# Performance work log

Measured on AMD Instinct MI355X. Metric: run time of the kernel, lower is better.

The kernel has to match this reference:

```python
import jax, jax.numpy as jnp
import numpy as np

OBS_LEN = 16; PRED_LEN = 25; N = 192; P = N * N; GH = GW = 8
IN_DIM = 2; OUT_DIM = 5; ENC = 64; DEC = 128
EMB = 32; DYN = 32; C1 = 64; C2 = 16; SOC = 3 * 3 * C2

def lrelu(x):
    return jnp.where(x >= 0, x, 0.1 * x)

def lstm_step(x, h, c, Wih, Whh, bih, bhh):
    # torch nn.LSTM gate order: i, f, g, o
    z = x @ Wih.T + h @ Whh.T + (bih + bhh)
    i, f, g, o = jnp.split(z, 4, axis=-1)
    c = jax.nn.sigmoid(f) * c + jax.nn.sigmoid(i) * jnp.tanh(g)
    h = jax.nn.sigmoid(o) * jnp.tanh(c)
    return h, c

def _indexed_lstm(frames, idxs, n_states, Wip, bip, Wih, Whh, bih, bhh):
    # per-frame gather of hidden/cell rows -> one LSTM step -> scatter back
    H0 = jnp.zeros((n_states, ENC), jnp.float32)
    C0 = jnp.zeros((n_states, ENC), jnp.float32)
    def step(carry, inp):
        Hs, Cs = carry
        frame, idx = inp
        h, c = Hs[idx], Cs[idx]                       # gather [M, ENC]
        emb = lrelu(frame @ Wip.T + bip)              # [M, EMB]
        h, c = lstm_step(emb, h, c, Wih, Whh, bih, bhh)
        return (Hs.at[idx].set(h), Cs.at[idx].set(c)), None  # scatter
    (Hs, _), _ = jax.lax.scan(step, (H0, C0), (frames, idxs))
    return Hs

def setup_inputs():
    key = jax.random.key(0)
    ks = jax.random.split(key, 16)
    def w(k, shape, fan):
        return (jax.random.normal(k, shape, jnp.float32) / np.sqrt(fan)).astype(jnp.float32)
    inp = {}
    inp['obs_traj'] = jax.random.normal(ks[0], (OBS_LEN, N, IN_DIM), jnp.float32)
    inp['obs_ngbrs_traj'] = jax.random.normal(ks[1], (OBS_LEN, P, IN_DIM), jnp.float32)
    inp['masks'] = jnp.ones((N, GH, GW, ENC), dtype=bool)  # fully occupied social grid
    inp['masks_idxs'] = jax.random.randint(ks[2], (N * GH * GW,), 0, P)
    inp['obs_traj_idxs'] = jnp.tile(jnp.arange(N), (OBS_LEN, 1))        # all nodes present each frame
    inp['obs_ngbrs_traj_idxs'] = jnp.tile(jnp.arange(P), (OBS_LEN, 1))  # all pair slots present
    inp['num_nodes'] = N
    inp['Wip'] = w(ks[3], (EMB, IN_DIM), IN_DIM); inp['bip'] = jnp.zeros((EMB,), jnp.float32)
    inp['Wih_e'] = w(ks[4], (4 * ENC, EMB), EMB); inp['Whh_e'] = w(ks[5], (4 * ENC, ENC), ENC)
    inp['bih_e'] = jnp.zeros((4 * ENC,), jnp.float32); inp['bhh_e'] = jnp.zeros((4 * ENC,), jnp.float32)
    inp['Wdyn'] = w(ks[6], (DYN, ENC), ENC); inp['bdyn'] = jnp.zeros((DYN,), jnp.float32)
    inp['Wc1'] = w(ks[7], (C1, ENC, 3, 3), ENC * 9); inp['bc1'] = jnp.zeros((C1,), jnp.float32)
    inp['Wc2'] = w(ks[8], (C2, C1, 3, 3), C1 * 9); inp['bc2'] = jnp.zeros((C2,), jnp.float32)
    inp['Wih_d'] = w(ks[9], (4 * DEC, SOC + DYN), SOC + DYN); inp['Whh_d'] = w(ks[10], (4 * DEC, DEC), DEC)
    inp['bih_d'] = jnp.zeros((4 * DEC,), jnp.float32); inp['bhh_d'] = jnp.zeros((4 * DEC,), jnp.float32)
    inp['Wop'] = w(ks[11], (OUT_DIM, DEC), DEC); inp['bop'] = jnp.zeros((OUT_DIM,), jnp.float32)
    return inp

def reference(obs_traj, obs_ngbrs_traj, masks, masks_idxs, obs_traj_idxs,
              obs_ngbrs_traj_idxs, num_nodes, Wip, bip, Wih_e, Whh_e, bih_e, bhh_e,
              Wdyn, bdyn, Wc1, bc1, Wc2, bc2, Wih_d, Whh_d, bih_d, bhh_d, Wop, bop):
    B = obs_traj_idxs.shape[1]
    # ego-trajectory encoder: per-frame indexed LSTM over num_nodes state slots
    Hs = _indexed_lstm(obs_traj, obs_traj_idxs, num_nodes, Wip, bip, Wih_e, Whh_e, bih_e, bhh_e)
    final_h = Hs[obs_traj_idxs[-1]]                   # [B, ENC]
    traj_enc = lrelu(final_h @ Wdyn.T + bdyn)         # [B, DYN]
    # neighbor-pair encoder: per-frame indexed LSTM over num_nodes^2 state slots
    Hn = _indexed_lstm(obs_ngbrs_traj, obs_ngbrs_traj_idxs, num_nodes * num_nodes,
                       Wip, bip, Wih_e, Whh_e, bih_e, bhh_e)
    ngbr_h = Hn[masks_idxs]                           # [B*GH*GW, ENC]
    # masked_scatter_ of neighbor encodings into fully-occupied social grid == reshape
    soc = jnp.where(masks, ngbr_h.reshape(B, GH, GW, ENC), 0.0)
    soc = jnp.transpose(soc, (0, 3, 2, 1))            # [B, ENC, GW, GH]
    dn = ('NCHW', 'OIHW', 'NCHW')
    soc = lrelu(jax.lax.conv_general_dilated(soc, Wc1, (1, 1), 'VALID', dimension_numbers=dn)
                + bc1[None, :, None, None])           # [B, C1, 6, 6]
    soc = lrelu(jax.lax.conv_general_dilated(soc, Wc2, (1, 1), 'VALID', dimension_numbers=dn)
                + bc2[None, :, None, None])           # [B, C2, 4, 4]
    soc = jax.lax.reduce_window(soc, -jnp.inf, jax.lax.max, (1, 1, 2, 2), (1, 1, 1, 1), 'VALID')
    soc = soc.reshape(B, SOC)                         # [B, 144]
    enc = jnp.concatenate([traj_enc, soc], axis=1)    # [B, DYN+SOC]
    h0 = jnp.zeros((B, DEC), jnp.float32); c0 = jnp.zeros((B, DEC), jnp.float32)
    def dec_step(carry, _):
        h, c = carry
        h, c = lstm_step(enc, h, c, Wih_d, Whh_d, bih_d, bhh_d)
        return (h, c), h
    _, hs = jax.lax.scan(dec_step, (h0, c0), None, length=PRED_LEN)
    o = hs @ Wop.T + bop                              # [PRED_LEN, B, 5]
    # bivariate Gaussian output activation (mu_x, mu_y, sigma_x, sigma_y, corr)
    return jnp.stack([o[..., 0], o[..., 1], jnp.exp(o[..., 2]),
                      jnp.exp(o[..., 3]), jnp.tanh(o[..., 4])], axis=-1)
```

## Files before the change

### kernel.cpp

```cpp
#include <hip/hip_runtime.h>
#include <hip/hip_bf16.h>

#define OBS_LEN 16
#define PRED_LEN 25
#define NNODES 192
#define PAIRS 36864
#define ENC 64
#define EMB 32
#define KTOT 96
#define DEC 128
#define SOCDYN 176
#define PAIR_GROUPS 2304
#define EGO_GROUPS 12
#define PREP_ELEMS 234496
#define HSTR 136

typedef short short8 __attribute__((ext_vector_type(8)));
typedef float f32x4 __attribute__((ext_vector_type(4)));

__device__ __forceinline__ float sigm(float x) {
    return __builtin_amdgcn_rcpf(1.f + __expf(-x));
}
__device__ __forceinline__ float tanh_f(float x) {
    return fmaf(-2.f, __builtin_amdgcn_rcpf(1.f + __expf(2.f * x)), 1.f);
}
__device__ __forceinline__ float lrelu(float x) { return (x >= 0.f) ? x : 0.1f * x; }

__device__ __forceinline__ unsigned short f2bf(float f) {
    union { float f; unsigned u; } v; v.f = f;
    unsigned r = v.u + 0x7fffu + ((v.u >> 16) & 1u);
    return (unsigned short)(r >> 16);
}
__device__ __forceinline__ float bf2f(unsigned short s) {
    union { unsigned u; float f; } v; v.u = ((unsigned)s) << 16; return v.f;
}

__global__ __launch_bounds__(1024, 1)
void prep_dedup_kernel(const float* __restrict__ Wih_d, const float* __restrict__ Whh_d,
                       const float* __restrict__ Wc1, const float* __restrict__ Wc2,
                       const float* __restrict__ Wih_e, const float* __restrict__ Whh_e,
                       const int* __restrict__ masks_idxs,
                       unsigned short* __restrict__ Whh_bf, unsigned short* __restrict__ Wih_bf,
                       unsigned short* __restrict__ WT1bf, unsigned short* __restrict__ WT2bf,
                       unsigned short* __restrict__ Wenc_bf,
                       int* __restrict__ list, int* __restrict__ list_count)
{
    const int t = threadIdx.x, b = blockIdx.x;
    if (b < 229) {
        int idx = b * 1024 + t;
        if (idx < 65536) {
            int m = idx >> 7, k = idx & 127;
            Whh_bf[idx] = f2bf(Whh_d[m * 128 + k]);
        } else if (idx < 65536 + 98304) {
            int i = idx - 65536;
            int m = i / 192, k = i % 192;
            Wih_bf[i] = (k < 176) ? f2bf(Wih_d[m * 176 + k]) : (unsigned short)0;
        } else if (idx < 65536 + 98304 + 36864) {
            int i = idx - (65536 + 98304);
            int o = i / 576, k = i % 576;
            int c = k / 9, tap = k % 9;
            WT1bf[i] = f2bf(Wc1[(o * 64 + c) * 9 + tap]);
        } else if (idx < 65536 + 98304 + 36864 + 9216) {
            int i = idx - (65536 + 98304 + 36864);
            int o = i / 576, k = i % 576;
            int c = k / 9, tap = k % 9;
            WT2bf[i] = f2bf(Wc2[(o * 64 + c) * 9 + tap]);
        } else if (idx < PREP_ELEMS) {
            int i = idx - (65536 + 98304 + 36864 + 9216);
            int m = i / 96, k = i % 96;
            Wenc_bf[i] = f2bf((k < 32) ? Wih_e[m * 32 + k] : Whh_e[m * 64 + (k - 32)]);
        }
        return;
    }
    __shared__ unsigned bm[1152];
    __shared__ int pcs[1024];
    for (int i = t; i < 1152; i += 1024) bm[i] = 0u;
    __syncthreads();
    for (int i = t; i < 12288; i += 1024) {
        const int r = masks_idxs[i];
        atomicOr(&bm[r >> 5], 1u << (r & 31));
    }
    __syncthreads();
    int pc = 0;
    if (t < 576) pc = __popc(bm[2 * t]) + __popc(bm[2 * t + 1]);
    pcs[t] = pc;
    __syncthreads();
    for (int ofs = 1; ofs < 1024; ofs <<= 1) {
        int v = (t >= ofs) ? pcs[t - ofs] : 0;
        __syncthreads();
        pcs[t] += v;
        __syncthreads();
    }
    if (t == 1023) list_count[0] = pcs[1023];
    if (t < 576) {
        int base = pcs[t] - pc;
#pragma unroll
        for (int wi = 0; wi < 2; ++wi) {
            unsigned wv = bm[2 * t + wi];
            const int rowbase = (2 * t + wi) * 32;
            while (wv) {
                const int bit = __ffs(wv) - 1;
                list[base++] = rowbase + bit;
                wv &= wv - 1;
            }
        }
    }
}

__global__ __launch_bounds__(256, 3)
void enc_lstm_kernel(const float* __restrict__ obs_traj,
                     const float* __restrict__ obs_ngbrs,
                     const float* __restrict__ Wip, const float* __restrict__ bip,
                     const unsigned short* __restrict__ Wenc_bf,
                     const float* __restrict__ bih, const float* __restrict__ bhh,
                     const int* __restrict__ list, const int* __restrict__ list_count,
                     float* __restrict__ Hn,
                     float* __restrict__ final_h)
{
    __shared__ __align__(16) short embs[16 * 16 * 40];
    __shared__ __align__(16) short hb[2][16 * 72];
    __shared__ int rows_s[16];

    const int t = threadIdx.x;
    const int wj = t >> 6, lane = t & 63, ln = lane & 15, kq = lane >> 4;
    const int b = blockIdx.x;
    const bool is_ego = (b >= PAIR_GROUPS);

    if (!is_ego) {
        const int cnt = list_count[0];
        if (b * 16 >= cnt) return;
        if (t < 16) rows_s[t] = list[min(b * 16 + t, cnt - 1)];
    } else {
        if (t < 16) rows_s[t] = (b - PAIR_GROUPS) * 16 + t;
    }

    short8 afrag[4][3];
#pragma unroll
    for (int g = 0; g < 4; ++g)
#pragma unroll
        for (int kc = 0; kc < 3; ++kc)
            afrag[g][kc] = *(const short8*)&Wenc_bf[(g * 64 + wj * 16 + ln) * 96 + kc * 32 + kq * 8];

    float bsv[4][4];
#pragma unroll
    for (int g = 0; g < 4; ++g)
#pragma unroll
        for (int r = 0; r < 4; ++r) {
            const int m = g * 64 + wj * 16 + kq * 4 + r;
            bsv[g][r] = bih[m] + bhh[m];
        }

    __syncthreads();

    {
        const int row = t & 15, stp = t >> 4;
        const int r = rows_s[row];
        const float* sp = is_ego ? (obs_traj + stp * NNODES * 2)
                                 : (obs_ngbrs + stp * PAIRS * 2);
        const float x0 = sp[r * 2 + 0];
        const float x1 = sp[r * 2 + 1];
        unsigned* dst = (unsigned*)&embs[(stp * 16 + row) * 40];
#pragma unroll
        for (int k = 0; k < 32; k += 2) {
            const float e0 = lrelu(fmaf(x0, Wip[2 * k + 0], fmaf(x1, Wip[2 * k + 1], bip[k])));
            const float e1 = lrelu(fmaf(x0, Wip[2 * k + 2], fmaf(x1, Wip[2 * k + 3], bip[k + 1])));
            dst[k >> 1] = (unsigned)f2bf(e0) | ((unsigned)f2bf(e1) << 16);
        }
    }
    for (int i = t; i < 2 * 16 * 72 / 2; i += 256) ((unsigned*)hb)[i] = 0u;
    __syncthreads();

    float cst[4] = {0.f, 0.f, 0.f, 0.f};
    int p = 0;
    for (int stp = 0; stp < OBS_LEN; ++stp) {
        const short8 bf0 = *(const short8*)&embs[(stp * 16 + ln) * 40 + kq * 8];
        const short* hbp = &hb[p][ln * 72 + kq * 8];
        const short8 bf1 = *(const short8*)hbp;
        const short8 bf2 = *(const short8*)(hbp + 32);
        f32x4 acc[4];
#pragma unroll
        for (int g = 0; g < 4; ++g) {
            f32x4 a = { bsv[g][0], bsv[g][1], bsv[g][2], bsv[g][3] };
            a = __builtin_amdgcn_mfma_f32_16x16x32_bf16(afrag[g][0], bf0, a, 0, 0, 0);
            a = __builtin_amdgcn_mfma_f32_16x16x32_bf16(afrag[g][1], bf1, a, 0, 0, 0);
            acc[g] = __builtin_amdgcn_mfma_f32_16x16x32_bf16(afrag[g][2], bf2, a, 0, 0, 0);
        }
        unsigned long long pk = 0;
#pragma unroll
        for (int r = 0; r < 4; ++r) {
            const float cn = fmaf(sigm(acc[1][r]), cst[r], sigm(acc[0][r]) * tanh_f(acc[2][r]));
            cst[r] = cn;
            const float h = sigm(acc[3][r]) * tanh_f(cn);
            pk |= (unsigned long long)f2bf(h) << (16 * r);
        }
        *(unsigned long long*)&hb[1 - p][ln * 72 + wj * 16 + kq * 4] = pk;
        p ^= 1;
        __syncthreads();
    }

    {
        const int row = t >> 4, k0 = (t & 15) * 4;
        unsigned long long pk = *(const unsigned long long*)&hb[p][row * 72 + k0];
        float4 v;
        v.x = bf2f((unsigned short)(pk));
        v.y = bf2f((unsigned short)(pk >> 16));
        v.z = bf2f((unsigned short)(pk >> 32));
        v.w = bf2f((unsigned short)(pk >> 48));
        float* dst = is_ego ? (final_h + rows_s[row] * 64 + k0)
                            : (Hn + (long)rows_s[row] * 64 + k0);
        *(float4*)dst = v;
    }
}

__global__ __launch_bounds__(256, 1)
void conv_kernel(const float* __restrict__ Hn, const int* __restrict__ masks_idxs,
                 const float* __restrict__ final_h, const float* __restrict__ Wdyn,
                 const float* __restrict__ bdyn,
                 const unsigned short* __restrict__ WT1bf, const float* __restrict__ bc1,
                 const unsigned short* __restrict__ WT2bf, const float* __restrict__ bc2,
                 float* __restrict__ enc)
{
    __shared__ __align__(16) short in2bf[64][72];
    __shared__ __align__(16) short imc1[48][584];
    __shared__ __align__(16) short s1bf[64][40];
    __shared__ __align__(16) short imc2[16][584];
    __shared__ __align__(16) float red[4][256];
    __shared__ float s2s[16 * 17];

    const int t = threadIdx.x, b = blockIdx.x;
    const int w = t >> 6, lane = t & 63, ln = lane & 15, kq = lane >> 4;

    short8 a1f[18];
#pragma unroll
    for (int kc = 0; kc < 18; ++kc)
        a1f[kc] = *(const short8*)&WT1bf[(w * 16 + ln) * 576 + kc * 32 + kq * 8];

    const int c2start = (w < 2) ? w * 5 : 10 + (w - 2) * 4;
    const int c2cnt = (w < 2) ? 5 : 4;
    short8 a2f[5];
#pragma unroll
    for (int i = 0; i < 5; ++i) {
        const int kc = c2start + min(i, c2cnt - 1);
        a2f[i] = *(const short8*)&WT2bf[ln * 576 + kc * 32 + kq * 8];
    }

    for (int i = 0; i < 16; ++i) {
        const int c = t & 63;
        const int p = (i << 2) + (t >> 6);
        const int u = p >> 3, v = p & 7;
        const int row = masks_idxs[b * 64 + v * 8 + u];
        in2bf[c][p] = (short)f2bf(Hn[(long)row * 64 + c]);
    }
    if (t < 32) {
        float acc = bdyn[t];
        for (int k = 0; k < 64; ++k) acc = fmaf(final_h[b * 64 + k], Wdyn[t * 64 + k], acc);
        enc[b * SOCDYN + t] = lrelu(acc);
    }
    __syncthreads();

    for (int i = t; i < 36 * 64; i += 256) {
        const int n = i >> 6, c = i & 63;
        const int x = n / 6, y = n % 6;
        short* dst = &imc1[n][c * 9];
#pragma unroll
        for (int dx = 0; dx < 3; ++dx)
#pragma unroll
            for (int dy = 0; dy < 3; ++dy)
                dst[dx * 3 + dy] = in2bf[c][(x + dx) * 8 + (y + dy)];
    }
    __syncthreads();

    {
        float bcv[4];
#pragma unroll
        for (int r = 0; r < 4; ++r) bcv[r] = bc1[w * 16 + kq * 4 + r];
#pragma unroll
        for (int nt = 0; nt < 3; ++nt) {
            f32x4 acc = { bcv[0], bcv[1], bcv[2], bcv[3] };
            const short* bp = &imc1[nt * 16 + ln][kq * 8];
#pragma unroll
            for (int kc = 0; kc < 18; ++kc) {
                const short8 bfr = *(const short8*)(bp + kc * 32);
                acc = __builtin_amdgcn_mfma_f32_16x16x32_bf16(a1f[kc], bfr, acc, 0, 0, 0);
            }
            const int n = nt * 16 + ln;
            if (n < 36) {
#pragma unroll
                for (int r = 0; r < 4; ++r)
                    s1bf[w * 16 + kq * 4 + r][n] = (short)f2bf(lrelu(acc[r]));
            }
        }
    }
    __syncthreads();

    for (int i = t; i < 16 * 64; i += 256) {
        const int n2 = i >> 6, c = i & 63;
        const int x = n2 >> 2, y = n2 & 3;
        short* dst = &imc2[n2][c * 9];
#pragma unroll
        for (int dx = 0; dx < 3; ++dx)
#pragma unroll
            for (int dy = 0; dy < 3; ++dy)
                dst[dx * 3 + dy] = s1bf[c][(x + dx) * 6 + (y + dy)];
    }
    __syncthreads();

    {
        f32x4 acc = { 0.f, 0.f, 0.f, 0.f };
        const short* bp = &imc2[ln][kq * 8];
#pragma unroll
        for (int i = 0; i < 5; ++i) {
            if (i < c2cnt) {
                const short8 bfr = *(const short8*)(bp + (c2start + i) * 32);
                acc = __builtin_amdgcn_mfma_f32_16x16x32_bf16(a2f[i], bfr, acc, 0, 0, 0);
            }
        }
        *(f32x4*)&red[w][lane * 4] = acc;
    }
    __syncthreads();

    {
        const float v = red[0][t] + red[1][t] + red[2][t] + red[3][t];
        const int l = t >> 2, r = t & 3;
        const int m = (l >> 4) * 4 + r, n = l & 15;
        s2s[m * 17 + n] = lrelu(v + bc2[m]);
    }
    __syncthreads();

    if (t < 144) {
        const int o = t / 9, ij = t % 9, i = ij / 3, j = ij % 3;
        const float v00 = s2s[o * 17 + i * 4 + j];
        const float v01 = s2s[o * 17 + i * 4 + j + 1];
        const float v10 = s2s[o * 17 + (i + 1) * 4 + j];
        const float v11 = s2s[o * 17 + (i + 1) * 4 + j + 1];
        enc[b * SOCDYN + 32 + t] = fmaxf(fmaxf(v00, v01), fmaxf(v10, v11));
    }
}

__global__ __launch_bounds__(512, 1)
void dec_kernel(const float* __restrict__ enc,
                const unsigned short* __restrict__ Wih_bf,
                const unsigned short* __restrict__ Whh_bf,
                const float* __restrict__ bih_d, const float* __restrict__ bhh_d,
                const float* __restrict__ Wop, const float* __restrict__ bop,
                float* __restrict__ out)
{
    __shared__ __align__(16) short encfr[3072];
    __shared__ __align__(16) short hist[PRED_LEN * 16 * HSTR];
    __shared__ float wop_s[5 * 128];

    const int t = threadIdx.x;
    const int w = t >> 6, lane = t & 63, ln = lane & 15, kq = lane >> 4;
    const int row0 = blockIdx.x * 16;

    for (int i = t; i < 3072; i += 512) {
        const int n = i / 192, k = i % 192;
        const float v = (k < 176) ? enc[(row0 + n) * SOCDYN + k] : 0.f;
        encfr[(k >> 3) * 128 + n * 8 + (k & 7)] = (short)f2bf(v);
    }
    for (int i = t; i < 640; i += 512) wop_s[i] = Wop[i];

    short8 wfrag[4][4];
#pragma unroll
    for (int g = 0; g < 4; ++g)
#pragma unroll
        for (int kc = 0; kc < 4; ++kc)
            wfrag[g][kc] = *(const short8*)&Whh_bf[(g * 128 + w * 16 + ln) * 128 + kc * 32 + kq * 8];

    f32x4 zin[4];
#pragma unroll
    for (int g = 0; g < 4; ++g)
#pragma unroll
        for (int r = 0; r < 4; ++r) {
            const int m = g * 128 + w * 16 + kq * 4 + r;
            zin[g][r] = bih_d[m] + bhh_d[m];
        }

    __syncthreads();

#pragma unroll
    for (int kc = 0; kc < 6; ++kc) {
        const short8 bfr = *(const short8*)&encfr[(kc * 4 + kq) * 128 + ln * 8];
#pragma unroll
        for (int g = 0; g < 4; ++g) {
            const short8 afr = *(const short8*)&Wih_bf[(g * 128 + w * 16 + ln) * 192 + kc * 32 + kq * 8];
            zin[g] = __builtin_amdgcn_mfma_f32_16x16x32_bf16(afr, bfr, zin[g], 0, 0, 0);
        }
    }

    float c4[4] = {0.f, 0.f, 0.f, 0.f};
    const int hb_wr = ln * HSTR + w * 16 + kq * 4;

    for (int stp = 0; stp < PRED_LEN; ++stp) {
        f32x4 z[4];
#pragma unroll
        for (int g = 0; g < 4; ++g) z[g] = zin[g];
        if (stp > 0) {
            const short* hp = &hist[(stp - 1) * 16 * HSTR + ln * HSTR + kq * 8];
            short8 bh[4];
#pragma unroll
            for (int kc = 0; kc < 4; ++kc)
                bh[kc] = *(const short8*)(hp + kc * 32);
#pragma unroll
            for (int kc = 0; kc < 4; ++kc)
#pragma unroll
                for (int g = 0; g < 4; ++g)
                    z[g] = __builtin_amdgcn_mfma_f32_16x16x32_bf16(wfrag[g][kc], bh[kc], z[g], 0, 0, 0);
        }
        unsigned long long pk = 0;
#pragma unroll
        for (int r = 0; r < 4; ++r) {
            const float cn = fmaf(sigm(z[1][r]), c4[r], sigm(z[0][r]) * tanh_f(z[2][r]));
            c4[r] = cn;
            const float h = sigm(z[3][r]) * tanh_f(cn);
            pk |= (unsigned long long)f2bf(h) << (16 * r);
        }
        *(unsigned long long*)&hist[stp * 16 * HSTR + hb_wr] = pk;
        __syncthreads();
    }

    for (int pi = t; pi < PRED_LEN * 16; pi += 512) {
        const int ts = pi >> 4, n = pi & 15;
        const short* hp = &hist[(ts * 16 + n) * HSTR];
        float a0 = bop[0], a1 = bop[1], a2 = bop[2], a3 = bop[3], a4 = bop[4];
#pragma unroll 4
        for (int kb = 0; kb < 16; ++kb) {
            const short8 h8 = *(const short8*)(hp + kb * 8);
#pragma unroll
            for (int q = 0; q < 8; ++q) {
                const float h = bf2f((unsigned short)h8[q]);
                const int k = kb * 8 + q;
                a0 = fmaf(h, wop_s[0 * 128 + k], a0);
                a1 = fmaf(h, wop_s[1 * 128 + k], a1);
                a2 = fmaf(h, wop_s[2 * 128 + k], a2);
                a3 = fmaf(h, wop_s[3 * 128 + k], a3);
                a4 = fmaf(h, wop_s[4 * 128 + k], a4);
            }
        }
        float* op = &out[((long)ts * NNODES + row0 + n) * 5];
        op[0] = a0;
        op[1] = a1;
        op[2] = __expf(a2);
        op[3] = __expf(a3);
        op[4] = tanh_f(a4);
    }
}

extern "C" void kernel_launch(void* const* d_in, const int* in_sizes, int n_in,
                              void* d_out, int out_size, void* d_ws, size_t ws_size,
                              hipStream_t stream) {
    const float* obs_traj   = (const float*)d_in[0];
    const float* obs_ngbrs  = (const float*)d_in[1];
    const int*   masks_idxs = (const int*)d_in[3];
    const float* Wip   = (const float*)d_in[7];
    const float* bip   = (const float*)d_in[8];
    const float* Wih_e = (const float*)d_in[9];
    const float* Whh_e = (const float*)d_in[10];
    const float* bih_e = (const float*)d_in[11];
    const float* bhh_e = (const float*)d_in[12];
    const float* Wdyn  = (const float*)d_in[13];
    const float* bdyn  = (const float*)d_in[14];
    const float* Wc1   = (const float*)d_in[15];
    const float* bc1   = (const float*)d_in[16];
    const float* Wc2   = (const float*)d_in[17];
    const float* bc2   = (const float*)d_in[18];
    const float* Wih_d = (const float*)d_in[19];
    const float* Whh_d = (const float*)d_in[20];
    const float* bih_d = (const float*)d_in[21];
    const float* bhh_d = (const float*)d_in[22];
    const float* Wop   = (const float*)d_in[23];
    const float* bop   = (const float*)d_in[24];
    float* out = (float*)d_out;

    float* ws = (float*)d_ws;
    float* Hn      = ws;
    float* final_h = Hn + 2359296;
    float* encb    = final_h + 12288;
    unsigned short* Whh_bf  = (unsigned short*)(encb + 33792);
    unsigned short* Wih_bf  = Whh_bf + 65536;
    unsigned short* WT1bf   = Wih_bf + 98304;
    unsigned short* WT2bf   = WT1bf + 36864;
    unsigned short* Wenc_bf = WT2bf + 9216;
    int*   list    = (int*)(Wenc_bf + 24576);
    int*   list_count = list + 36864;

    hipLaunchKernelGGL(prep_dedup_kernel, dim3(230), dim3(1024), 0, stream,
                       Wih_d, Whh_d, Wc1, Wc2, Wih_e, Whh_e, masks_idxs,
                       Whh_bf, Wih_bf, WT1bf, WT2bf, Wenc_bf, list, list_count);
    hipLaunchKernelGGL(enc_lstm_kernel, dim3(PAIR_GROUPS + EGO_GROUPS), dim3(256), 0, stream,
                       obs_traj, obs_ngbrs, Wip, bip, Wenc_bf, bih_e, bhh_e,
                       list, list_count, Hn, final_h);
    hipLaunchKernelGGL(conv_kernel, dim3(NNODES), dim3(256), 0, stream,
                       Hn, masks_idxs, final_h, Wdyn, bdyn, WT1bf, bc1, WT2bf, bc2, encb);
    hipLaunchKernelGGL(dec_kernel, dim3(NNODES / 16), dim3(512), 0, stream,
                       encb, Wih_bf, Whh_bf, bih_d, bhh_d, Wop, bop, out);
}
```

Baseline: 194.7 us.

## Restructure encoder LSTM to single-wave blocks and fold weight conversion into consumers

The encoder LSTM now runs one 64-lane wave per 16-row group. That wave computes all 256 gate rows and keeps the whole recurrence in registers, which removes the per-step block barrier and the shared embedding buffer. The separate weight-to-bf16 prep pass is gone: each kernel converts fp32 weights to bf16 on the fly while loading fragments, leaving dedup as a single small block. Exp calls now use exp2 with a log2e scale. The trade-off is heavy register use (48 weight fragments per lane), fewer waves per group, and repeated fp32 weight loads and conversions in every block.

```diff
diff --git a/kernel.cpp b/kernel.cpp
--- a/kernel.cpp
+++ b/kernel.cpp
@@ -7,22 +7,24 @@
 #define PAIRS 36864
 #define ENC 64
 #define EMB 32
-#define KTOT 96
 #define DEC 128
 #define SOCDYN 176
 #define PAIR_GROUPS 2304
 #define EGO_GROUPS 12
-#define PREP_ELEMS 234496
 #define HSTR 136
+#define LOG2E 1.4426950408889634f
 
 typedef short short8 __attribute__((ext_vector_type(8)));
 typedef float f32x4 __attribute__((ext_vector_type(4)));
 
 __device__ __forceinline__ float sigm(float x) {
-    return __builtin_amdgcn_rcpf(1.f + __expf(-x));
+    return __builtin_amdgcn_rcpf(1.f + __builtin_amdgcn_exp2f(-LOG2E * x));
 }
 __device__ __forceinline__ float tanh_f(float x) {
-    return fmaf(-2.f, __builtin_amdgcn_rcpf(1.f + __expf(2.f * x)), 1.f);
+    return fmaf(-2.f, __builtin_amdgcn_rcpf(1.f + __builtin_amdgcn_exp2f((2.f * LOG2E) * x)), 1.f);
+}
+__device__ __forceinline__ float expf_fast(float x) {
+    return __builtin_amdgcn_exp2f(LOG2E * x);
 }
 __device__ __forceinline__ float lrelu(float x) { return (x >= 0.f) ? x : 0.1f * x; }
 
@@ -36,44 +38,12 @@
 }
 
 __global__ __launch_bounds__(1024, 1)
-void prep_dedup_kernel(const float* __restrict__ Wih_d, const float* __restrict__ Whh_d,
-                       const float* __restrict__ Wc1, const float* __restrict__ Wc2,
-                       const float* __restrict__ Wih_e, const float* __restrict__ Whh_e,
-                       const int* __restrict__ masks_idxs,
-                       unsigned short* __restrict__ Whh_bf, unsigned short* __restrict__ Wih_bf,
-                       unsigned short* __restrict__ WT1bf, unsigned short* __restrict__ WT2bf,
-                       unsigned short* __restrict__ Wenc_bf,
-                       int* __restrict__ list, int* __restrict__ list_count)
+void dedup_kernel(const int* __restrict__ masks_idxs,
+                  int* __restrict__ list, int* __restrict__ list_count)
 {
-    const int t = threadIdx.x, b = blockIdx.x;
-    if (b < 229) {
-        int idx = b * 1024 + t;
-        if (idx < 65536) {
-            int m = idx >> 7, k = idx & 127;
-            Whh_bf[idx] = f2bf(Whh_d[m * 128 + k]);
-        } else if (idx < 65536 + 98304) {
-            int i = idx - 65536;
-            int m = i / 192, k = i % 192;
-            Wih_bf[i] = (k < 176) ? f2bf(Wih_d[m * 176 + k]) : (unsigned short)0;
-        } else if (idx < 65536 + 98304 + 36864) {
-            int i = idx - (65536 + 98304);
-            int o = i / 576, k = i % 576;
-            int c = k / 9, tap = k % 9;
-            WT1bf[i] = f2bf(Wc1[(o * 64 + c) * 9 + tap]);
-        } else if (idx < 65536 + 98304 + 36864 + 9216) {
-            int i = idx - (65536 + 98304 + 36864);
-            int o = i / 576, k = i % 576;
-            int c = k / 9, tap = k % 9;
-            WT2bf[i] = f2bf(Wc2[(o * 64 + c) * 9 + tap]);
-        } else if (idx < PREP_ELEMS) {
-            int i = idx - (65536 + 98304 + 36864 + 9216);
-            int m = i / 96, k = i % 96;
-            Wenc_bf[i] = f2bf((k < 32) ? Wih_e[m * 32 + k] : Whh_e[m * 64 + (k - 32)]);
-        }
-        return;
-    }
     __shared__ unsigned bm[1152];
     __shared__ int pcs[1024];
+    const int t = threadIdx.x;
     for (int i = t; i < 1152; i += 1024) bm[i] = 0u;
     __syncthreads();
     for (int i = t; i < 12288; i += 1024) {
@@ -107,108 +77,136 @@
     }
 }
 
-__global__ __launch_bounds__(256, 3)
+__global__ __launch_bounds__(64, 1)
 void enc_lstm_kernel(const float* __restrict__ obs_traj,
                      const float* __restrict__ obs_ngbrs,
                      const float* __restrict__ Wip, const float* __restrict__ bip,
-                     const unsigned short* __restrict__ Wenc_bf,
+                     const float* __restrict__ Wih_e,
+                     const float* __restrict__ Whh_e,
                      const float* __restrict__ bih, const float* __restrict__ bhh,
                      const int* __restrict__ list, const int* __restrict__ list_count,
                      float* __restrict__ Hn,
                      float* __restrict__ final_h)
 {
-    __shared__ __align__(16) short embs[16 * 16 * 40];
-    __shared__ __align__(16) short hb[2][16 * 72];
-    __shared__ int rows_s[16];
-
-    const int t = threadIdx.x;
-    const int wj = t >> 6, lane = t & 63, ln = lane & 15, kq = lane >> 4;
+    __shared__ __align__(16) short hw[16 * 72];
+    __shared__ __align__(16) float xs[OBS_LEN][16][2];
+
+    const int lane = threadIdx.x;
+    const int ln = lane & 15, kq = lane >> 4;
     const int b = blockIdx.x;
     const bool is_ego = (b >= PAIR_GROUPS);
-
+    int cnt = 0;
     if (!is_ego) {
-        const int cnt = list_count[0];
+        cnt = list_count[0];
         if (b * 16 >= cnt) return;
-        if (t < 16) rows_s[t] = list[min(b * 16 + t, cnt - 1)];
-    } else {
-        if (t < 16) rows_s[t] = (b - PAIR_GROUPS) * 16 + t;
-    }
-
-    short8 afrag[4][3];
+    }
+    const int myrow = is_ego ? ((b - PAIR_GROUPS) * 16 + ln)
+                             : list[min(b * 16 + ln, cnt - 1)];
+
+    {
+        const float* sp = is_ego ? obs_traj : obs_ngbrs;
+        const int stride = is_ego ? (NNODES * 2) : (PAIRS * 2);
+#pragma unroll
+        for (int i = 0; i < 4; ++i) {
+            const int s = kq * 4 + i;
+            const float* p = sp + (long)s * stride + (long)myrow * 2;
+            xs[s][ln][0] = p[0];
+            xs[s][ln][1] = p[1];
+        }
+    }
+
+    float w0[8], w1[8], bb[8];
+#pragma unroll
+    for (int jj = 0; jj < 8; ++jj) {
+        const int k = kq * 8 + jj;
+        w0[jj] = Wip[2 * k];
+        w1[jj] = Wip[2 * k + 1];
+        bb[jj] = bip[k];
+    }
+
+    short8 af[4][4][3];
+    float bsv[4][4][4];
 #pragma unroll
     for (int g = 0; g < 4; ++g)
 #pragma unroll
-        for (int kc = 0; kc < 3; ++kc)
-            afrag[g][kc] = *(const short8*)&Wenc_bf[(g * 64 + wj * 16 + ln) * 96 + kc * 32 + kq * 8];
-
-    float bsv[4][4];
-#pragma unroll
-    for (int g = 0; g < 4; ++g)
-#pragma unroll
-        for (int r = 0; r < 4; ++r) {
-            const int m = g * 64 + wj * 16 + kq * 4 + r;
-            bsv[g][r] = bih[m] + bhh[m];
-        }
-
-    __syncthreads();
+        for (int jt = 0; jt < 4; ++jt) {
+            const int m = g * 64 + jt * 16 + ln;
+#pragma unroll
+            for (int kc = 0; kc < 3; ++kc) {
+                const float* wp = (kc == 0) ? (Wih_e + m * 32 + kq * 8)
+                                            : (Whh_e + m * 64 + (kc - 1) * 32 + kq * 8);
+                short8 a;
+#pragma unroll
+                for (int j = 0; j < 8; ++j) a[j] = (short)f2bf(wp[j]);
+                af[g][jt][kc] = a;
+            }
+            const int mb = g * 64 + jt * 16 + kq * 4;
+#pragma unroll
+            for (int r = 0; r < 4; ++r) bsv[g][jt][r] = bih[mb + r] + bhh[mb + r];
+        }
+
+    float cst[4][4];
+#pragma unroll
+    for (int jt = 0; jt < 4; ++jt)
+#pragma unroll
+        for (int r = 0; r < 4; ++r) cst[jt][r] = 0.f;
+
+    short8 hf1, hf2;
+#pragma unroll
+    for (int j = 0; j < 8; ++j) { hf1[j] = 0; hf2[j] = 0; }
+
+    for (int s = 0; s < OBS_LEN; ++s) {
+        const float x0 = xs[s][ln][0], x1 = xs[s][ln][1];
+        short8 be;
+#pragma unroll
+        for (int jj = 0; jj < 8; ++jj) {
+            const float e = lrelu(fmaf(x0, w0[jj], fmaf(x1, w1[jj], bb[jj])));
+            be[jj] = (short)f2bf(e);
+        }
+#pragma unroll
+        for (int jt = 0; jt < 4; ++jt) {
+            f32x4 acc[4];
+#pragma unroll
+            for (int g = 0; g < 4; ++g) {
+                f32x4 a = { bsv[g][jt][0], bsv[g][jt][1], bsv[g][jt][2], bsv[g][jt][3] };
+                a = __builtin_amdgcn_mfma_f32_16x16x32_bf16(af[g][jt][0], be, a, 0, 0, 0);
+                a = __builtin_amdgcn_mfma_f32_16x16x32_bf16(af[g][jt][1], hf1, a, 0, 0, 0);
+                acc[g] = __builtin_amdgcn_mfma_f32_16x16x32_bf16(af[g][jt][2], hf2, a, 0, 0, 0);
+            }
+            unsigned long long pk = 0;
+#pragma unroll
+            for (int r = 0; r < 4; ++r) {
+                const float cn = fmaf(sigm(acc[1][r]), cst[jt][r],
+                                      sigm(acc[0][r]) * tanh_f(acc[2][r]));
+                cst[jt][r] = cn;
+                const float h = sigm(acc[3][r]) * tanh_f(cn);
+                pk |= (unsigned long long)f2bf(h) << (16 * r);
+            }
+            *(unsigned long long*)&hw[ln * 72 + jt * 16 + kq * 4] = pk;
+        }
+        hf1 = *(const short8*)&hw[ln * 72 + kq * 8];
+        hf2 = *(const short8*)&hw[ln * 72 + 32 + kq * 8];
+    }
 
     {
-        const int row = t & 15, stp = t >> 4;
-        const int r = rows_s[row];
-        const float* sp = is_ego ? (obs_traj + stp * NNODES * 2)
-                                 : (obs_ngbrs + stp * PAIRS * 2);
-        const float x0 = sp[r * 2 + 0];
-        const float x1 = sp[r * 2 + 1];
-        unsigned* dst = (unsigned*)&embs[(stp * 16 + row) * 40];
-#pragma unroll
-        for (int k = 0; k < 32; k += 2) {
-            const float e0 = lrelu(fmaf(x0, Wip[2 * k + 0], fmaf(x1, Wip[2 * k + 1], bip[k])));
-            const float e1 = lrelu(fmaf(x0, Wip[2 * k + 2], fmaf(x1, Wip[2 * k + 3], bip[k + 1])));
-            dst[k >> 1] = (unsigned)f2bf(e0) | ((unsigned)f2bf(e1) << 16);
-        }
-    }
-    for (int i = t; i < 2 * 16 * 72 / 2; i += 256) ((unsigned*)hb)[i] = 0u;
-    __syncthreads();
-
-    float cst[4] = {0.f, 0.f, 0.f, 0.f};
-    int p = 0;
-    for (int stp = 0; stp < OBS_LEN; ++stp) {
-        const short8 bf0 = *(const short8*)&embs[(stp * 16 + ln) * 40 + kq * 8];
-        const short* hbp = &hb[p][ln * 72 + kq * 8];
-        const short8 bf1 = *(const short8*)hbp;
-        const short8 bf2 = *(const short8*)(hbp + 32);
-        f32x4 acc[4];
-#pragma unroll
-        for (int g = 0; g < 4; ++g) {
-            f32x4 a = { bsv[g][0], bsv[g][1], bsv[g][2], bsv[g][3] };
-            a = __builtin_amdgcn_mfma_f32_16x16x32_bf16(afrag[g][0], bf0, a, 0, 0, 0);
-            a = __builtin_amdgcn_mfma_f32_16x16x32_bf16(afrag[g][1], bf1, a, 0, 0, 0);
-            acc[g] = __builtin_amdgcn_mfma_f32_16x16x32_bf16(afrag[g][2], bf2, a, 0, 0, 0);
-        }
-        unsigned long long pk = 0;
-#pragma unroll
-        for (int r = 0; r < 4; ++r) {
-            const float cn = fmaf(sigm(acc[1][r]), cst[r], sigm(acc[0][r]) * tanh_f(acc[2][r]));
-            cst[r] = cn;
-            const float h = sigm(acc[3][r]) * tanh_f(cn);
-            pk |= (unsigned long long)f2bf(h) << (16 * r);
-        }
-        *(unsigned long long*)&hb[1 - p][ln * 72 + wj * 16 + kq * 4] = pk;
-        p ^= 1;
-        __syncthreads();
-    }
-
-    {
-        const int row = t >> 4, k0 = (t & 15) * 4;
-        unsigned long long pk = *(const unsigned long long*)&hb[p][row * 72 + k0];
-        float4 v;
-        v.x = bf2f((unsigned short)(pk));
-        v.y = bf2f((unsigned short)(pk >> 16));
-        v.z = bf2f((unsigned short)(pk >> 32));
-        v.w = bf2f((unsigned short)(pk >> 48));
-        float* dst = is_ego ? (final_h + rows_s[row] * 64 + k0)
-                            : (Hn + (long)rows_s[row] * 64 + k0);
-        *(float4*)dst = v;
+        const int rr = lane >> 2, q = lane & 3;
+        const int row2 = is_ego ? ((b - PAIR_GROUPS) * 16 + rr)
+                                : list[min(b * 16 + rr, cnt - 1)];
+        float* dst = is_ego ? (final_h + (long)row2 * 64 + q * 16)
+                            : (Hn + (long)row2 * 64 + q * 16);
+        const short8 ha = *(const short8*)&hw[rr * 72 + q * 16];
+        const short8 hb2 = *(const short8*)&hw[rr * 72 + q * 16 + 8];
+        float vals[16];
+#pragma unroll
+        for (int j = 0; j < 8; ++j) {
+            vals[j] = bf2f((unsigned short)ha[j]);
+            vals[8 + j] = bf2f((unsigned short)hb2[j]);
+        }
+#pragma unroll
+        for (int j = 0; j < 4; ++j) {
+            float4 vv = { vals[4 * j], vals[4 * j + 1], vals[4 * j + 2], vals[4 * j + 3] };
+            *(float4*)(dst + 4 * j) = vv;
+        }
     }
 }
 
@@ -216,8 +214,8 @@
 void conv_kernel(const float* __restrict__ Hn, const int* __restrict__ masks_idxs,
                  const float* __restrict__ final_h, const float* __restrict__ Wdyn,
                  const float* __restrict__ bdyn,
-                 const unsigned short* __restrict__ WT1bf, const float* __restrict__ bc1,
-                 const unsigned short* __restrict__ WT2bf, const float* __restrict__ bc2,
+                 const float* __restrict__ Wc1, const float* __restrict__ bc1,
+                 const float* __restrict__ Wc2, const float* __restrict__ bc2,
                  float* __restrict__ enc)
 {
     __shared__ __align__(16) short in2bf[64][72];
@@ -232,8 +230,13 @@
 
     short8 a1f[18];
 #pragma unroll
-    for (int kc = 0; kc < 18; ++kc)
-        a1f[kc] = *(const short8*)&WT1bf[(w * 16 + ln) * 576 + kc * 32 + kq * 8];
+    for (int kc = 0; kc < 18; ++kc) {
+        const float* wp = Wc1 + (w * 16 + ln) * 576 + kc * 32 + kq * 8;
+        short8 a;
+#pragma unroll
+        for (int j = 0; j < 8; ++j) a[j] = (short)f2bf(wp[j]);
+        a1f[kc] = a;
+    }
 
     const int c2start = (w < 2) ? w * 5 : 10 + (w - 2) * 4;
     const int c2cnt = (w < 2) ? 5 : 4;
@@ -241,7 +244,11 @@
 #pragma unroll
     for (int i = 0; i < 5; ++i) {
         const int kc = c2start + min(i, c2cnt - 1);
-        a2f[i] = *(const short8*)&WT2bf[ln * 576 + kc * 32 + kq * 8];
+        const float* wp = Wc2 + ln * 576 + kc * 32 + kq * 8;
+        short8 a;
+#pragma unroll
+        for (int j = 0; j < 8; ++j) a[j] = (short)f2bf(wp[j]);
+        a2f[i] = a;
     }
 
     for (int i = 0; i < 16; ++i) {
@@ -339,8 +346,8 @@
 
 __global__ __launch_bounds__(512, 1)
 void dec_kernel(const float* __restrict__ enc,
-                const unsigned short* __restrict__ Wih_bf,
-                const unsigned short* __restrict__ Whh_bf,
+                const float* __restrict__ Wih_d,
+                const float* __restrict__ Whh_d,
                 const float* __restrict__ bih_d, const float* __restrict__ bhh_d,
                 const float* __restrict__ Wop, const float* __restrict__ bop,
                 float* __restrict__ out)
@@ -364,8 +371,13 @@
 #pragma unroll
     for (int g = 0; g < 4; ++g)
 #pragma unroll
-        for (int kc = 0; kc < 4; ++kc)
-            wfrag[g][kc] = *(const short8*)&Whh_bf[(g * 128 + w * 16 + ln) * 128 + kc * 32 + kq * 8];
+        for (int kc = 0; kc < 4; ++kc) {
+            const float* wp = Whh_d + (g * 128 + w * 16 + ln) * 128 + kc * 32 + kq * 8;
+            short8 a;
+#pragma unroll
+            for (int j = 0; j < 8; ++j) a[j] = (short)f2bf(wp[j]);
+            wfrag[g][kc] = a;
+        }
 
     f32x4 zin[4];
 #pragma unroll
@@ -381,9 +393,18 @@
 #pragma unroll
     for (int kc = 0; kc < 6; ++kc) {
         const short8 bfr = *(const short8*)&encfr[(kc * 4 + kq) * 128 + ln * 8];
+        const int kk = kc * 32 + kq * 8;
 #pragma unroll
         for (int g = 0; g < 4; ++g) {
-            const short8 afr = *(const short8*)&Wih_bf[(g * 128 + w * 16 + ln) * 192 + kc * 32 + kq * 8];
+            short8 afr;
+            if (kk < 176) {
+                const float* wp = Wih_d + (g * 128 + w * 16 + ln) * 176 + kk;
+#pragma unroll
+                for (int j = 0; j < 8; ++j) afr[j] = (short)f2bf(wp[j]);
+            } else {
+#pragma unroll
+                for (int j = 0; j < 8; ++j) afr[j] = 0;
+            }
             zin[g] = __builtin_amdgcn_mfma_f32_16x16x32_bf16(afr, bfr, zin[g], 0, 0, 0);
         }
     }
@@ -440,8 +461,8 @@
         float* op = &out[((long)ts * NNODES + row0 + n) * 5];
         op[0] = a0;
         op[1] = a1;
-        op[2] = __expf(a2);
-        op[3] = __expf(a3);
+        op[2] = expf_fast(a2);
+        op[3] = expf_fast(a3);
         op[4] = tanh_f(a4);
     }
 }
@@ -476,22 +497,16 @@
     float* Hn      = ws;
     float* final_h = Hn + 2359296;
     float* encb    = final_h + 12288;
-    unsigned short* Whh_bf  = (unsigned short*)(encb + 33792);
-    unsigned short* Wih_bf  = Whh_bf + 65536;
-    unsigned short* WT1bf   = Wih_bf + 98304;
-    unsigned short* WT2bf   = WT1bf + 36864;
-    unsigned short* Wenc_bf = WT2bf + 9216;
-    int*   list    = (int*)(Wenc_bf + 24576);
+    int*   list    = (int*)(encb + 33792);
     int*   list_count = list + 36864;
 
-    hipLaunchKernelGGL(prep_dedup_kernel, dim3(230), dim3(1024), 0, stream,
-                       Wih_d, Whh_d, Wc1, Wc2, Wih_e, Whh_e, masks_idxs,
-                       Whh_bf, Wih_bf, WT1bf, WT2bf, Wenc_bf, list, list_count);
-    hipLaunchKernelGGL(enc_lstm_kernel, dim3(PAIR_GROUPS + EGO_GROUPS), dim3(256), 0, stream,
-                       obs_traj, obs_ngbrs, Wip, bip, Wenc_bf, bih_e, bhh_e,
+    hipLaunchKernelGGL(dedup_kernel, dim3(1), dim3(1024), 0, stream,
+                       masks_idxs, list, list_count);
+    hipLaunchKernelGGL(enc_lstm_kernel, dim3(PAIR_GROUPS + EGO_GROUPS), dim3(64), 0, stream,
+                       obs_traj, obs_ngbrs, Wip, bip, Wih_e, Whh_e, bih_e, bhh_e,
                        list, list_count, Hn, final_h);
     hipLaunchKernelGGL(conv_kernel, dim3(NNODES), dim3(256), 0, stream,
-                       Hn, masks_idxs, final_h, Wdyn, bdyn, WT1bf, bc1, WT2bf, bc2, encb);
+                       Hn, masks_idxs, final_h, Wdyn, bdyn, Wc1, bc1, Wc2, bc2, encb);
     hipLaunchKernelGGL(dec_kernel, dim3(NNODES / 16), dim3(512), 0, stream,
-                       encb, Wih_bf, Whh_bf, bih_d, bhh_d, Wop, bop, out);
-}
+                       encb, Wih_d, Whh_d, bih_d, bhh_d, Wop, bop, out);
+}
```

Result: slower. 216.9 us (+11.4%).

## Replace conv im2col with implicit tap-indexed GEMM, split decoder MFMA chains

Applied to the files above, without the earlier changes.

The conv kernel drops the explicit im2col staging buffers and instead reads B fragments straight from transposed channel-last LDS tiles, indexed by tap. Conv weights are reordered in prep to match a tap-major layout. Occupancy hint goes to 2 blocks per CU now that LDS use is smaller. The decoder recurrence splits each gate's MFMA accumulation into two independent chains to shorten dependency latency, and the exp/sigmoid/tanh helpers use exp2 directly. The changes cut LDS traffic, barriers and serial MFMA latency, at the cost of some extra bank-conflict risk on the strided tap reads.

```diff
diff --git a/kernel.cpp b/kernel.cpp
--- a/kernel.cpp
+++ b/kernel.cpp
@@ -7,22 +7,25 @@
 #define PAIRS 36864
 #define ENC 64
 #define EMB 32
-#define KTOT 96
 #define DEC 128
 #define SOCDYN 176
 #define PAIR_GROUPS 2304
 #define EGO_GROUPS 12
 #define PREP_ELEMS 234496
 #define HSTR 136
+#define LOG2E 1.4426950408889634f
 
 typedef short short8 __attribute__((ext_vector_type(8)));
 typedef float f32x4 __attribute__((ext_vector_type(4)));
 
 __device__ __forceinline__ float sigm(float x) {
-    return __builtin_amdgcn_rcpf(1.f + __expf(-x));
+    return __builtin_amdgcn_rcpf(1.f + __builtin_amdgcn_exp2f(-LOG2E * x));
 }
 __device__ __forceinline__ float tanh_f(float x) {
-    return fmaf(-2.f, __builtin_amdgcn_rcpf(1.f + __expf(2.f * x)), 1.f);
+    return fmaf(-2.f, __builtin_amdgcn_rcpf(1.f + __builtin_amdgcn_exp2f((2.f * LOG2E) * x)), 1.f);
+}
+__device__ __forceinline__ float expf_fast(float x) {
+    return __builtin_amdgcn_exp2f(LOG2E * x);
 }
 __device__ __forceinline__ float lrelu(float x) { return (x >= 0.f) ? x : 0.1f * x; }
 
@@ -57,13 +60,11 @@
             Wih_bf[i] = (k < 176) ? f2bf(Wih_d[m * 176 + k]) : (unsigned short)0;
         } else if (idx < 65536 + 98304 + 36864) {
             int i = idx - (65536 + 98304);
-            int o = i / 576, k = i % 576;
-            int c = k / 9, tap = k % 9;
+            int tap = i >> 12, o = (i >> 6) & 63, c = i & 63;
             WT1bf[i] = f2bf(Wc1[(o * 64 + c) * 9 + tap]);
         } else if (idx < 65536 + 98304 + 36864 + 9216) {
             int i = idx - (65536 + 98304 + 36864);
-            int o = i / 576, k = i % 576;
-            int c = k / 9, tap = k % 9;
+            int tap = i >> 10, o = (i >> 6) & 15, c = i & 63;
             WT2bf[i] = f2bf(Wc2[(o * 64 + c) * 9 + tap]);
         } else if (idx < PREP_ELEMS) {
             int i = idx - (65536 + 98304 + 36864 + 9216);
@@ -212,7 +213,7 @@
     }
 }
 
-__global__ __launch_bounds__(256, 1)
+__global__ __launch_bounds__(256, 2)
 void conv_kernel(const float* __restrict__ Hn, const int* __restrict__ masks_idxs,
                  const float* __restrict__ final_h, const float* __restrict__ Wdyn,
                  const float* __restrict__ bdyn,
@@ -220,28 +221,29 @@
                  const unsigned short* __restrict__ WT2bf, const float* __restrict__ bc2,
                  float* __restrict__ enc)
 {
-    __shared__ __align__(16) short in2bf[64][72];
-    __shared__ __align__(16) short imc1[48][584];
-    __shared__ __align__(16) short s1bf[64][40];
-    __shared__ __align__(16) short imc2[16][584];
+    __shared__ __align__(16) short in2T[64][72];
+    __shared__ __align__(16) short s1T[36][72];
     __shared__ __align__(16) float red[4][256];
     __shared__ float s2s[16 * 17];
 
     const int t = threadIdx.x, b = blockIdx.x;
     const int w = t >> 6, lane = t & 63, ln = lane & 15, kq = lane >> 4;
 
-    short8 a1f[18];
-#pragma unroll
-    for (int kc = 0; kc < 18; ++kc)
-        a1f[kc] = *(const short8*)&WT1bf[(w * 16 + ln) * 576 + kc * 32 + kq * 8];
-
-    const int c2start = (w < 2) ? w * 5 : 10 + (w - 2) * 4;
-    const int c2cnt = (w < 2) ? 5 : 4;
+    short8 a1f[9][2];
+#pragma unroll
+    for (int tap = 0; tap < 9; ++tap)
+#pragma unroll
+        for (int kc = 0; kc < 2; ++kc)
+            a1f[tap][kc] = *(const short8*)&WT1bf[(tap * 64 + w * 16 + ln) * 64 + kc * 32 + kq * 8];
+
+    const int p2start = (w < 2) ? w * 5 : 10 + (w - 2) * 4;
+    const int p2cnt = (w < 2) ? 5 : 4;
     short8 a2f[5];
 #pragma unroll
     for (int i = 0; i < 5; ++i) {
-        const int kc = c2start + min(i, c2cnt - 1);
-        a2f[i] = *(const short8*)&WT2bf[ln * 576 + kc * 32 + kq * 8];
+        const int pi = p2start + min(i, p2cnt - 1);
+        const int tap = pi >> 1, kc = pi & 1;
+        a2f[i] = *(const short8*)&WT2bf[(tap * 16 + ln) * 64 + kc * 32 + kq * 8];
     }
 
     for (int i = 0; i < 16; ++i) {
@@ -249,7 +251,7 @@
         const int p = (i << 2) + (t >> 6);
         const int u = p >> 3, v = p & 7;
         const int row = masks_idxs[b * 64 + v * 8 + u];
-        in2bf[c][p] = (short)f2bf(Hn[(long)row * 64 + c]);
+        in2T[p][c] = (short)f2bf(Hn[(long)row * 64 + c]);
     }
     if (t < 32) {
         float acc = bdyn[t];
@@ -258,60 +260,46 @@
     }
     __syncthreads();
 
-    for (int i = t; i < 36 * 64; i += 256) {
-        const int n = i >> 6, c = i & 63;
-        const int x = n / 6, y = n % 6;
-        short* dst = &imc1[n][c * 9];
-#pragma unroll
-        for (int dx = 0; dx < 3; ++dx)
-#pragma unroll
-            for (int dy = 0; dy < 3; ++dy)
-                dst[dx * 3 + dy] = in2bf[c][(x + dx) * 8 + (y + dy)];
-    }
-    __syncthreads();
-
     {
         float bcv[4];
 #pragma unroll
         for (int r = 0; r < 4; ++r) bcv[r] = bc1[w * 16 + kq * 4 + r];
 #pragma unroll
         for (int nt = 0; nt < 3; ++nt) {
+            const int n = min(nt * 16 + ln, 35);
+            const int x = n / 6, y = n % 6;
             f32x4 acc = { bcv[0], bcv[1], bcv[2], bcv[3] };
-            const short* bp = &imc1[nt * 16 + ln][kq * 8];
-#pragma unroll
-            for (int kc = 0; kc < 18; ++kc) {
-                const short8 bfr = *(const short8*)(bp + kc * 32);
-                acc = __builtin_amdgcn_mfma_f32_16x16x32_bf16(a1f[kc], bfr, acc, 0, 0, 0);
-            }
-            const int n = nt * 16 + ln;
-            if (n < 36) {
+#pragma unroll
+            for (int tap = 0; tap < 9; ++tap) {
+                const int dx = tap / 3, dy = tap % 3;
+                const short* bp = &in2T[(x + dx) * 8 + (y + dy)][kq * 8];
+#pragma unroll
+                for (int kc = 0; kc < 2; ++kc) {
+                    const short8 bfr = *(const short8*)(bp + kc * 32);
+                    acc = __builtin_amdgcn_mfma_f32_16x16x32_bf16(a1f[tap][kc], bfr, acc, 0, 0, 0);
+                }
+            }
+            if (nt * 16 + ln < 36) {
+                unsigned long long pk = 0;
 #pragma unroll
                 for (int r = 0; r < 4; ++r)
-                    s1bf[w * 16 + kq * 4 + r][n] = (short)f2bf(lrelu(acc[r]));
-            }
-        }
-    }
-    __syncthreads();
-
-    for (int i = t; i < 16 * 64; i += 256) {
-        const int n2 = i >> 6, c = i & 63;
-        const int x = n2 >> 2, y = n2 & 3;
-        short* dst = &imc2[n2][c * 9];
-#pragma unroll
-        for (int dx = 0; dx < 3; ++dx)
-#pragma unroll
-            for (int dy = 0; dy < 3; ++dy)
-                dst[dx * 3 + dy] = s1bf[c][(x + dx) * 6 + (y + dy)];
+                    pk |= (unsigned long long)f2bf(lrelu(acc[r])) << (16 * r);
+                *(unsigned long long*)&s1T[n][w * 16 + kq * 4] = pk;
+            }
+        }
     }
     __syncthreads();
 
     {
+        const int x = ln >> 2, y = ln & 3;
         f32x4 acc = { 0.f, 0.f, 0.f, 0.f };
-        const short* bp = &imc2[ln][kq * 8];
 #pragma unroll
         for (int i = 0; i < 5; ++i) {
-            if (i < c2cnt) {
-                const short8 bfr = *(const short8*)(bp + (c2start + i) * 32);
+            if (i < p2cnt) {
+                const int pi = p2start + i;
+                const int tap = pi >> 1, kc = pi & 1;
+                const int dx = tap / 3, dy = tap % 3;
+                const short8 bfr = *(const short8*)&s1T[(x + dx) * 6 + (y + dy)][kc * 32 + kq * 8];
                 acc = __builtin_amdgcn_mfma_f32_16x16x32_bf16(a2f[i], bfr, acc, 0, 0, 0);
             }
         }
@@ -401,11 +389,19 @@
 #pragma unroll
             for (int kc = 0; kc < 4; ++kc)
                 bh[kc] = *(const short8*)(hp + kc * 32);
-#pragma unroll
-            for (int kc = 0; kc < 4; ++kc)
-#pragma unroll
-                for (int g = 0; g < 4; ++g)
-                    z[g] = __builtin_amdgcn_mfma_f32_16x16x32_bf16(wfrag[g][kc], bh[kc], z[g], 0, 0, 0);
+            f32x4 zb[4];
+#pragma unroll
+            for (int g = 0; g < 4; ++g) {
+                f32x4 zero = { 0.f, 0.f, 0.f, 0.f };
+                z[g] = __builtin_amdgcn_mfma_f32_16x16x32_bf16(wfrag[g][0], bh[0], z[g], 0, 0, 0);
+                zb[g] = __builtin_amdgcn_mfma_f32_16x16x32_bf16(wfrag[g][2], bh[2], zero, 0, 0, 0);
+                z[g] = __builtin_amdgcn_mfma_f32_16x16x32_bf16(wfrag[g][1], bh[1], z[g], 0, 0, 0);
+                zb[g] = __builtin_amdgcn_mfma_f32_16x16x32_bf16(wfrag[g][3], bh[3], zb[g], 0, 0, 0);
+            }
+#pragma unroll
+            for (int g = 0; g < 4; ++g)
+#pragma unroll
+                for (int r = 0; r < 4; ++r) z[g][r] += zb[g][r];
         }
         unsigned long long pk = 0;
 #pragma unroll
@@ -440,8 +436,8 @@
         float* op = &out[((long)ts * NNODES + row0 + n) * 5];
         op[0] = a0;
         op[1] = a1;
-        op[2] = __expf(a2);
-        op[3] = __expf(a3);
+        op[2] = expf_fast(a2);
+        op[3] = expf_fast(a3);
         op[4] = tanh_f(a4);
     }
 }
```

Result: faster. 190.3 us (-2.2%).
